# Kernel optimization log

Measured on AMD Instinct MI355X. Metric: run time of the kernel, lower is better.

Reference implementation:

```python
import jax, jax.numpy as jnp
import numpy as np

B, S, D = 4, 16, 512          # batch, seq, attention_dim
V, T = 32000, 18              # vocab_size, tree_depth
INNER = V - 1                 # internal nodes of Huffman tree


def setup_inputs() -> dict:
    key = jax.random.key(0)
    k_att, k_w, k_idx, k_bit = jax.random.split(key, 4)
    att = jax.random.normal(k_att, (B, S, D), dtype=jnp.float32)
    weight = jax.random.normal(k_w, (INNER, D), dtype=jnp.float32) * 0.02
    path_index = jax.random.randint(k_idx, (V * T,), 0, INNER, dtype=jnp.int64)
    # left/right branch bits: sign=+1,bias=0 -> p ; sign=-1,bias=1 -> 1-p
    bits = jax.random.randint(k_bit, (V * T,), 0, 2).astype(jnp.float32)
    path_sign = 1.0 - 2.0 * bits
    path_bias = bits
    return {
        "att": att,
        "weight": weight,
        "path_index": path_index,
        "path_sign": path_sign,
        "path_bias": path_bias,
        "vocab_size": V,
        "tree_depth": T,
    }


def reference(att, weight, path_index, path_sign, path_bias, vocab_size, tree_depth):
    # h: sigmoid of linear projection onto internal-node vectors  [B,S,INNER]
    h = jax.nn.sigmoid(jnp.einsum("bsd,nd->bsn", att, weight))
    # gather per-(token,depth) internal-node probs, flip via sign/bias
    g = jnp.take(h, path_index, axis=-1) * path_sign + path_bias  # [B,S,V*T]
    Hm = g.reshape(att.shape[0], -1, vocab_size, tree_depth)      # [B,S,V,T]
    return jnp.sum(jnp.log(Hm), axis=-1)                          # [B,S,V]
```

## Files before the change

### kernel.cpp

```cpp
#include <hip/hip_runtime.h>
#include <hip/hip_bf16.h>

#define BS    64
#define DDIM  512
#define NV    32000
#define TD    18
#define INNER 31999
#define ROWP  32000

typedef __attribute__((ext_vector_type(8))) short short8;
typedef __attribute__((ext_vector_type(4))) float floatx4;

__device__ __forceinline__ float bf16_to_f32(unsigned short u) {
    union { unsigned int i; float f; } v; v.i = ((unsigned int)u) << 16; return v.f;
}
__device__ __forceinline__ unsigned short f32_to_bf16(float f) {
    union { float f; unsigned int i; } v; v.f = f;
    unsigned int r = v.i + 0x7FFFu + ((v.i >> 16) & 1u);
    return (unsigned short)(r >> 16);
}

#define IDXB 2250
__global__ __launch_bounds__(256) void prep(
    const int* __restrict__ idx,
    const unsigned int* __restrict__ signbits,
    unsigned short* __restrict__ idx2T,
    const float4* __restrict__ att,
    ushort4* __restrict__ attb)
{
    const int b = blockIdx.x;
    if (b < IDXB) {
        const unsigned int* w = (const unsigned int*)idx;
        bool i64 = true;
#pragma unroll
        for (int j = 1; j < 16; j += 2) i64 &= (w[j] == 0u);
        int o = b * 256 + threadIdx.x;
        int t = o / NV, v = o - t * NV;
        int i = v * TD + t;
        int val = i64 ? idx[2 * i] : idx[i];
        idx2T[o] = (unsigned short)((val << 1) | (int)(signbits[i] >> 31));
    } else {
        int i = (b - IDXB) * 256 + threadIdx.x;
        float4 a = att[i];
        ushort4 r;
        r.x = f32_to_bf16(a.x); r.y = f32_to_bf16(a.y);
        r.z = f32_to_bf16(a.z); r.w = f32_to_bf16(a.w);
        attb[i] = r;
    }
}

__global__ __launch_bounds__(256) void gemm_logsig(
    const unsigned short* __restrict__ attb,
    const float* __restrict__ weight,
    unsigned int* __restrict__ pairs)
{
    const int lane = threadIdx.x & 63;
    const int wave = threadIdx.x >> 6;
    const int nb   = blockIdx.x * 64 + wave * 16;
    const int l15  = lane & 15;
    const int quad = lane >> 4;

    floatx4 acc[4];
#pragma unroll
    for (int i = 0; i < 4; ++i) acc[i] = (floatx4){0.f, 0.f, 0.f, 0.f};

    int brow = nb + l15;
    if (brow > INNER - 1) brow = INNER - 1;
    const float*          bbase = weight + (size_t)brow * DDIM + quad * 8;
    const unsigned short* abase = attb + l15 * DDIM + quad * 8;

#pragma unroll 4
    for (int k0 = 0; k0 < DDIM; k0 += 32) {
        float4 b0 = *(const float4*)(bbase + k0);
        float4 b1 = *(const float4*)(bbase + k0 + 4);
        short8 bfrag;
        bfrag[0] = (short)f32_to_bf16(b0.x); bfrag[1] = (short)f32_to_bf16(b0.y);
        bfrag[2] = (short)f32_to_bf16(b0.z); bfrag[3] = (short)f32_to_bf16(b0.w);
        bfrag[4] = (short)f32_to_bf16(b1.x); bfrag[5] = (short)f32_to_bf16(b1.y);
        bfrag[6] = (short)f32_to_bf16(b1.z); bfrag[7] = (short)f32_to_bf16(b1.w);
#pragma unroll
        for (int mt = 0; mt < 4; ++mt) {
            short8 afrag = *(const short8*)(abase + mt * 16 * DDIM + k0);
            acc[mt] = __builtin_amdgcn_mfma_f32_16x16x32_bf16(afrag, bfrag, acc[mt], 0, 0, 0);
        }
    }

    const int n = nb + l15;
    if (n < INNER) {
#pragma unroll
        for (int mt = 0; mt < 4; ++mt) {
#pragma unroll
            for (int r = 0; r < 4; ++r) {
                const int m = mt * 16 + quad * 4 + r;
                float x = acc[mt][r];
                float lp = -(fmaxf(-x, 0.f) + __logf(1.f + __expf(-fabsf(x))));
                float lm = lp - x;
                pairs[m * ROWP + n] = (unsigned int)f32_to_bf16(lp)
                                    | ((unsigned int)f32_to_bf16(lm) << 16);
            }
        }
    }
}

__global__ __launch_bounds__(1024) void gather_pairs(
    const unsigned int* __restrict__ pairs,
    const unsigned short* __restrict__ idx2T,
    float* __restrict__ out)
{
    extern __shared__ unsigned int lds32[];
    const int bs    = blockIdx.y;
    const int vbase = blockIdx.x * 8000;
    const int tid   = threadIdx.x;

    const uint4* src = (const uint4*)(pairs + (size_t)bs * ROWP);
    for (int i = tid; i < ROWP / 4; i += 1024) ((uint4*)lds32)[i] = src[i];
    __syncthreads();

#pragma unroll
    for (int s = 0; s < 8; ++s) {
        int r = s * 1024 + tid;
        if (r < 8000) {
            const unsigned short* col = idx2T + vbase + r;
            float sum = 0.f;
#pragma unroll
            for (int t = 0; t < TD; ++t) {
                unsigned int e = col[(size_t)t * NV];
                unsigned int p = lds32[e >> 1];
                unsigned short h = (e & 1u) ? (unsigned short)(p >> 16)
                                            : (unsigned short)(p & 0xFFFFu);
                sum += bf16_to_f32(h);
            }
            out[bs * NV + vbase + r] = sum;
        }
    }
}

extern "C" void kernel_launch(void* const* d_in, const int* in_sizes, int n_in,
                              void* d_out, int out_size, void* d_ws, size_t ws_size,
                              hipStream_t stream)
{
    const float*        att    = (const float*)d_in[0];
    const float*        weight = (const float*)d_in[1];
    const int*          pidx   = (const int*)d_in[2];
    const unsigned int* psign  = (const unsigned int*)d_in[3];
    float* out = (float*)d_out;

    char* ws = (char*)d_ws;
    unsigned int*   pairs = (unsigned int*)ws;
    unsigned short* idx2T = (unsigned short*)(ws + 8192000);
    ushort4*        attb  = (ushort4*)       (ws + 9344000);

    hipFuncSetAttribute(reinterpret_cast<const void*>(gather_pairs),
                        hipFuncAttributeMaxDynamicSharedMemorySize, ROWP * 4);

    prep<<<IDXB + 32, 256, 0, stream>>>(pidx, psign, idx2T, (const float4*)att, attb);
    gemm_logsig<<<500, 256, 0, stream>>>((const unsigned short*)attb, weight, pairs);
    gather_pairs<<<dim3(4, BS), 1024, ROWP * 4, stream>>>(pairs, idx2T, out);
}
```

Baseline: 145.6 us.

## Transpose pair table to node-major and gather all 64 rows per index

The GEMM now writes the log-sigmoid pair table node-major ([node][64 rows]) with vectorized 16-byte stores, and the index table is kept in its original token-major order. The gather kernel has each wave read one 256-byte node row per path index, covering all 64 batch-seq rows at once, instead of staging a full 128 KB row in LDS per block and rereading the indices 64 times. A small LDS tile transposes the results for coalesced output writes. This trades LDS-resident random lookups for global/L2 random row reads of 256 bytes each.

```diff
diff --git a/kernel.cpp b/kernel.cpp
--- a/kernel.cpp
+++ b/kernel.cpp
@@ -1,12 +1,10 @@
 #include <hip/hip_runtime.h>
-#include <hip/hip_bf16.h>
 
 #define BS    64
 #define DDIM  512
 #define NV    32000
 #define TD    18
 #define INNER 31999
-#define ROWP  32000
 
 typedef __attribute__((ext_vector_type(8))) short short8;
 typedef __attribute__((ext_vector_type(4))) float floatx4;
@@ -24,7 +22,7 @@
 __global__ __launch_bounds__(256) void prep(
     const int* __restrict__ idx,
     const unsigned int* __restrict__ signbits,
-    unsigned short* __restrict__ idx2T,
+    unsigned short* __restrict__ idx2,
     const float4* __restrict__ att,
     ushort4* __restrict__ attb)
 {
@@ -35,10 +33,8 @@
 #pragma unroll
         for (int j = 1; j < 16; j += 2) i64 &= (w[j] == 0u);
         int o = b * 256 + threadIdx.x;
-        int t = o / NV, v = o - t * NV;
-        int i = v * TD + t;
-        int val = i64 ? idx[2 * i] : idx[i];
-        idx2T[o] = (unsigned short)((val << 1) | (int)(signbits[i] >> 31));
+        int val = i64 ? idx[2 * o] : idx[o];
+        idx2[o] = (unsigned short)((val << 1) | (int)(signbits[o] >> 31));
     } else {
         int i = (b - IDXB) * 256 + threadIdx.x;
         float4 a = att[i];
@@ -52,7 +48,7 @@
 __global__ __launch_bounds__(256) void gemm_logsig(
     const unsigned short* __restrict__ attb,
     const float* __restrict__ weight,
-    unsigned int* __restrict__ pairs)
+    unsigned int* __restrict__ pairsT)
 {
     const int lane = threadIdx.x & 63;
     const int wave = threadIdx.x >> 6;
@@ -87,52 +83,65 @@
 
     const int n = nb + l15;
     if (n < INNER) {
+        unsigned int* dst = pairsT + ((size_t)n << 6) + quad * 4;
 #pragma unroll
         for (int mt = 0; mt < 4; ++mt) {
+            unsigned int wds[4];
 #pragma unroll
             for (int r = 0; r < 4; ++r) {
-                const int m = mt * 16 + quad * 4 + r;
                 float x = acc[mt][r];
                 float lp = -(fmaxf(-x, 0.f) + __logf(1.f + __expf(-fabsf(x))));
                 float lm = lp - x;
-                pairs[m * ROWP + n] = (unsigned int)f32_to_bf16(lp)
-                                    | ((unsigned int)f32_to_bf16(lm) << 16);
+                wds[r] = (unsigned int)f32_to_bf16(lp)
+                       | ((unsigned int)f32_to_bf16(lm) << 16);
             }
+            uint4 wv; wv.x = wds[0]; wv.y = wds[1]; wv.z = wds[2]; wv.w = wds[3];
+            *(uint4*)(dst + mt * 16) = wv;
         }
     }
 }
 
-__global__ __launch_bounds__(1024) void gather_pairs(
-    const unsigned int* __restrict__ pairs,
-    const unsigned short* __restrict__ idx2T,
+__global__ __launch_bounds__(256) void gather_bs(
+    const unsigned int* __restrict__ pairsT,
+    const unsigned short* __restrict__ idx2,
     float* __restrict__ out)
 {
-    extern __shared__ unsigned int lds32[];
-    const int bs    = blockIdx.y;
-    const int vbase = blockIdx.x * 8000;
-    const int tid   = threadIdx.x;
+    __shared__ float tile[32][65];
+    const int lane  = threadIdx.x & 63;
+    const int wave  = threadIdx.x >> 6;
+    const int vbase = blockIdx.x * 32;
 
-    const uint4* src = (const uint4*)(pairs + (size_t)bs * ROWP);
-    for (int i = tid; i < ROWP / 4; i += 1024) ((uint4*)lds32)[i] = src[i];
+#pragma unroll
+    for (int i = 0; i < 8; ++i) {
+        const int vloc = wave * 8 + i;
+        const unsigned short* col = idx2 + (size_t)(vbase + vloc) * TD;
+        float s0 = 0.f, s1 = 0.f;
+#pragma unroll
+        for (int t = 0; t < TD; t += 2) {
+            unsigned int e0 = col[t];
+            unsigned int e1 = col[t + 1];
+            unsigned int p0 = pairsT[((size_t)(e0 >> 1) << 6) + lane];
+            unsigned int p1 = pairsT[((size_t)(e1 >> 1) << 6) + lane];
+            unsigned short h0 = (e0 & 1u) ? (unsigned short)(p0 >> 16)
+                                          : (unsigned short)(p0 & 0xFFFFu);
+            unsigned short h1 = (e1 & 1u) ? (unsigned short)(p1 >> 16)
+                                          : (unsigned short)(p1 & 0xFFFFu);
+            s0 += bf16_to_f32(h0);
+            s1 += bf16_to_f32(h1);
+        }
+        tile[vloc][lane] = s0 + s1;
+    }
     __syncthreads();
 
-#pragma unroll
-    for (int s = 0; s < 8; ++s) {
-        int r = s * 1024 + tid;
-        if (r < 8000) {
-            const unsigned short* col = idx2T + vbase + r;
-            float sum = 0.f;
-#pragma unroll
-            for (int t = 0; t < TD; ++t) {
-                unsigned int e = col[(size_t)t * NV];
-                unsigned int p = lds32[e >> 1];
-                unsigned short h = (e & 1u) ? (unsigned short)(p >> 16)
-                                            : (unsigned short)(p & 0xFFFFu);
-                sum += bf16_to_f32(h);
-            }
-            out[bs * NV + vbase + r] = sum;
-        }
-    }
+    const int bs  = threadIdx.x >> 2;
+    const int seg = threadIdx.x & 3;
+    float4 r0, r1;
+    r0.x = tile[seg * 8 + 0][bs]; r0.y = tile[seg * 8 + 1][bs];
+    r0.z = tile[seg * 8 + 2][bs]; r0.w = tile[seg * 8 + 3][bs];
+    r1.x = tile[seg * 8 + 4][bs]; r1.y = tile[seg * 8 + 5][bs];
+    r1.z = tile[seg * 8 + 6][bs]; r1.w = tile[seg * 8 + 7][bs];
+    float4* dst = (float4*)(out + (size_t)bs * NV + vbase + seg * 8);
+    dst[0] = r0; dst[1] = r1;
 }
 
 extern "C" void kernel_launch(void* const* d_in, const int* in_sizes, int n_in,
@@ -146,14 +155,11 @@
     float* out = (float*)d_out;
 
     char* ws = (char*)d_ws;
-    unsigned int*   pairs = (unsigned int*)ws;
-    unsigned short* idx2T = (unsigned short*)(ws + 8192000);
-    ushort4*        attb  = (ushort4*)       (ws + 9344000);
+    unsigned int*   pairsT = (unsigned int*)ws;
+    unsigned short* idx2   = (unsigned short*)(ws + 8192000);
+    ushort4*        attb   = (ushort4*)       (ws + 9344000);
 
-    hipFuncSetAttribute(reinterpret_cast<const void*>(gather_pairs),
-                        hipFuncAttributeMaxDynamicSharedMemorySize, ROWP * 4);
-
-    prep<<<IDXB + 32, 256, 0, stream>>>(pidx, psign, idx2T, (const float4*)att, attb);
-    gemm_logsig<<<500, 256, 0, stream>>>((const unsigned short*)attb, weight, pairs);
-    gather_pairs<<<dim3(4, BS), 1024, ROWP * 4, stream>>>(pairs, idx2T, out);
+    prep<<<IDXB + 32, 256, 0, stream>>>(pidx, psign, idx2, (const float4*)att, attb);
+    gemm_logsig<<<500, 256, 0, stream>>>((const unsigned short*)attb, weight, pairsT);
+    gather_bs<<<1000, 256, 0, stream>>>(pairsT, idx2, out);
 }
```

Measured after the change: 138.5 us. 1.05x faster.
